# Kernel optimization log

Hardware: AMD Instinct MI355X
Metric: run time of the kernel (lower is better)

## Reference

```python
import jax, jax.numpy as jnp
import numpy as np
import math

V, D, H, L, DFF = 32000, 1024, 16, 4, 4096
B, T_TGT, T_SRC = 4, 512, 512


def setup_inputs() -> dict:
    key = jax.random.key(0)
    ks = iter(jax.random.split(key, 64))
    s = 0.02
    inp = {
        'tgt': jax.random.randint(next(ks), (B, T_TGT), 0, V, dtype=jnp.int32),
        'encoder_output': jax.random.normal(next(ks), (B, T_SRC, D), jnp.float32),
        'tgt_mask': jnp.tril(jnp.ones((T_TGT, T_TGT), jnp.int32)),
        'emb': jax.random.normal(next(ks), (V, D)) * s,
        'Wout': jax.random.normal(next(ks), (D, V)) * s,
        'bout': jnp.zeros((V,)),
    }
    for pfx in ('s', 'c'):  # self / cross attention
        for nm in ('q', 'k', 'v', 'o'):
            inp[f'W{nm}_{pfx}'] = jax.random.normal(next(ks), (L, D, D)) * s
            inp[f'b{nm}_{pfx}'] = jnp.zeros((L, D))
    inp['W1'] = jax.random.normal(next(ks), (L, D, DFF)) * s
    inp['b1'] = jnp.zeros((L, DFF))
    inp['W2'] = jax.random.normal(next(ks), (L, DFF, D)) * s
    inp['b2'] = jnp.zeros((L, D))
    for i in (1, 2, 3):
        inp[f'ln{i}_g'] = jnp.ones((L, D))
        inp[f'ln{i}_b'] = jnp.zeros((L, D))
    return inp


def _layernorm(x, g, b, eps=1e-5):
    m = x.mean(-1, keepdims=True)
    v = ((x - m) ** 2).mean(-1, keepdims=True)
    return g * (x - m) * jax.lax.rsqrt(v + eps) + b


def _mha(xq, xkv, Wq, bq, Wk, bk, Wv, bv, Wo, bo, mask):
    Bq, Tq, Dm = xq.shape
    dk = Dm // H
    q = (xq @ Wq + bq).reshape(Bq, Tq, H, dk).transpose(0, 2, 1, 3)   # bhqd
    k = (xkv @ Wk + bk).reshape(Bq, -1, H, dk).transpose(0, 2, 1, 3)  # bhkd
    v = (xkv @ Wv + bv).reshape(Bq, -1, H, dk).transpose(0, 2, 1, 3)
    scores = jnp.einsum('bhqd,bhkd->bhqk', q, k) / math.sqrt(dk)
    if mask is not None:
        scores = jnp.where(mask[None, None] == 0, -1e9, scores)
    w = jax.nn.softmax(scores, axis=-1)                               # dropout: eval mode
    o = jnp.einsum('bhqk,bhkd->bhqd', w, v).transpose(0, 2, 1, 3).reshape(Bq, Tq, Dm)
    return o @ Wo + bo, w


def _pos_encoding(T, Dm):
    pos = jnp.arange(T, dtype=jnp.float32)[:, None]
    div = jnp.exp(jnp.arange(0, Dm, 2, dtype=jnp.float32) * (-math.log(10000.0) / Dm))
    pe = jnp.zeros((T, Dm))
    pe = pe.at[:, 0::2].set(jnp.sin(pos * div))
    pe = pe.at[:, 1::2].set(jnp.cos(pos * div))
    return pe


def reference(tgt, encoder_output, tgt_mask, emb, Wout, bout,
              Wq_s, bq_s, Wk_s, bk_s, Wv_s, bv_s, Wo_s, bo_s,
              Wq_c, bq_c, Wk_c, bk_c, Wv_c, bv_c, Wo_c, bo_c,
              W1, b1, W2, b2, ln1_g, ln1_b, ln2_g, ln2_b, ln3_g, ln3_b):
    x = emb[tgt] * math.sqrt(D) + _pos_encoding(tgt.shape[1], D)[None]
    self_ws, cross_ws = [], []
    for i in range(L):
        a1, sw = _mha(x, x, Wq_s[i], bq_s[i], Wk_s[i], bk_s[i], Wv_s[i], bv_s[i],
                      Wo_s[i], bo_s[i], tgt_mask)
        x = _layernorm(x + a1, ln1_g[i], ln1_b[i])
        a2, cw = _mha(x, encoder_output, Wq_c[i], bq_c[i], Wk_c[i], bk_c[i],
                      Wv_c[i], bv_c[i], Wo_c[i], bo_c[i], None)
        x = _layernorm(x + a2, ln2_g[i], ln2_b[i])
        ffn = jax.nn.relu(x @ W1[i] + b1[i]) @ W2[i] + b2[i]
        x = _layernorm(x + ffn, ln3_g[i], ln3_b[i])
        self_ws.append(sw)
        cross_ws.append(cw)
    logits = x @ Wout + bout
    return logits, jnp.stack(self_ws), jnp.stack(cross_ws)
```

## Files before the change

kernel.cpp:

```cpp
#include <hip/hip_runtime.h>


typedef unsigned short u16;
typedef __bf16 v8bf __attribute__((ext_vector_type(8)));
typedef float v4f __attribute__((ext_vector_type(4)));

namespace {
constexpr int kB = 4, kT = 512, kD = 1024, kH = 16, kDK = 64, kF = 4096, kV = 32000, kL = 4;
constexpr int kM = kB * kT;
constexpr long kTD = (long)kT * kD;
constexpr long kTT = (long)kT * kT;
constexpr long kHTT = (long)kH * kTT;
constexpr long kBHTT = (long)kB * kHTT;
constexpr long kLOG = (long)kM * kV;
constexpr long kPART = (long)kM * kD;
}

__device__ __forceinline__ u16 f2bf(float f) {
  union { float f; unsigned u; } v; v.f = f;
  unsigned r = v.u + 0x7FFFu + ((v.u >> 16) & 1u);
  return (u16)(r >> 16);
}
__device__ __forceinline__ float bf2f(u16 h) {
  union { unsigned u; float f; } v; v.u = ((unsigned)h) << 16;
  return v.f;
}

typedef __attribute__((address_space(3))) void lds_void;
typedef const __attribute__((address_space(1))) void glob_void;
__device__ __forceinline__ void gl2lds16(const void* g, void* l) {
  __builtin_amdgcn_global_load_lds((glob_void*)g, (lds_void*)l, 16, 0, 0);
}

template <int BM, int BN, int OUTBF, int VTR>
__global__ __launch_bounds__(256)
void gemm_bf(const u16* __restrict__ A0, const u16* __restrict__ B0,
             const float* __restrict__ bias, void* __restrict__ Cv,
             u16* __restrict__ vtw,
             const int K, const int lda, const int ldb, const int ldc,
             const int nH, const long sAb, const long sAh,
             const long sBb, const long sBh, const long sCb, const long sCh,
             const float scale, const int relu, const int bstride) {
  static_assert(BM % 32 == 0 && BN % 32 == 0, "tiles");
  __shared__ u16 As[2][BM][64];
  __shared__ u16 Bs[2][BN][64];
  const int tid = threadIdx.x;
  const int lane = tid & 63;
  const int w = tid >> 6;
  const int z = blockIdx.z;
  const int zb = z / nH, zh = z - zb * nH;
  const u16* A = A0 + zb * sAb + zh * sAh + (long)blockIdx.y * BM * lda;
  const u16* B = B0 + zb * sBb + zh * sBh + (long)blockIdx.x * BN * ldb;
  const long offC = zb * sCb + zh * sCh;
  const int wm = w >> 1, wn = w & 1;
  constexpr int FM = BM / 32, FN = BN / 32;
  v4f acc[FM][FN];
  const v4f zero = {0.f, 0.f, 0.f, 0.f};
#pragma unroll
  for (int i = 0; i < FM; ++i)
#pragma unroll
    for (int j = 0; j < FN; ++j) acc[i][j] = zero;
  const int l15 = lane & 15, lk = lane >> 4;
  const int lr8 = lane >> 3;
  const int swz = ((lane & 7) ^ lr8) * 8;
  const int l7 = l15 & 7;

#pragma unroll
  for (int s = 0; s < BM / 32; ++s)
    gl2lds16(A + (long)(w * (BM / 4) + s * 8 + lr8) * lda + swz,
             &As[0][w * (BM / 4) + s * 8][0]);
#pragma unroll
  for (int s = 0; s < BN / 32; ++s)
    gl2lds16(B + (long)(w * (BN / 4) + s * 8 + lr8) * ldb + swz,
             &Bs[0][w * (BN / 4) + s * 8][0]);

  const int NT = K >> 6;
  for (int kt = 0; kt < NT; ++kt) {
    const int cur = kt & 1;
    __syncthreads();
    if (kt + 1 < NT) {
      const int k0 = (kt + 1) << 6;
#pragma unroll
      for (int s = 0; s < BM / 32; ++s)
        gl2lds16(A + (long)(w * (BM / 4) + s * 8 + lr8) * lda + k0 + swz,
                 &As[cur ^ 1][w * (BM / 4) + s * 8][0]);
#pragma unroll
      for (int s = 0; s < BN / 32; ++s)
        gl2lds16(B + (long)(w * (BN / 4) + s * 8 + lr8) * ldb + k0 + swz,
                 &Bs[cur ^ 1][w * (BN / 4) + s * 8][0]);
    }
#pragma unroll
    for (int t = 0; t < 2; ++t) {
      const int c0 = t * 4;
      v8bf af[FM], bfr[FN];
#pragma unroll
      for (int i = 0; i < FM; ++i)
        af[i] = *(const v8bf*)&As[cur][wm * (BM / 2) + i * 16 + l15][((c0 + lk) ^ l7) * 8];
#pragma unroll
      for (int j = 0; j < FN; ++j)
        bfr[j] = *(const v8bf*)&Bs[cur][wn * (BN / 2) + j * 16 + l15][((c0 + lk) ^ l7) * 8];
#pragma unroll
      for (int i = 0; i < FM; ++i)
#pragma unroll
        for (int j = 0; j < FN; ++j)
          acc[i][j] = __builtin_amdgcn_mfma_f32_16x16x32_bf16(af[i], bfr[j], acc[i][j], 0, 0, 0);
    }
  }

  const long m0 = (long)blockIdx.y * BM + wm * (BM / 2);
  const int n0 = blockIdx.x * BN + wn * (BN / 2);
#pragma unroll
  for (int j = 0; j < FN; ++j) {
    const int col = n0 + j * 16 + l15;
    const float bv = (bias && zb == 0) ? bias[zh * bstride + col] : 0.0f;
#pragma unroll
    for (int i = 0; i < FM; ++i) {
      const long row = m0 + i * 16 + lk * 4;
#pragma unroll
      for (int r = 0; r < 4; ++r) {
        float v = acc[i][j][r] * scale + bv;
        if (relu) v = fmaxf(v, 0.0f);
        const long idx = offC + (row + r) * ldc + col;
        if (OUTBF) ((u16*)Cv)[idx] = f2bf(v);
        else       ((float*)Cv)[idx] = v;
        if (VTR) {
          const int colS = (int)(offC % 3072) + col;
          if (colS >= 2048) {
            const int hh = (colS - 2048) >> 6, dd = (colS - 2048) & 63;
            const int rowg = (int)(row + r);
            vtw[((long)((rowg >> 9) * 16 + hh)) * 32768 + dd * 512 + (rowg & 511)] = f2bf(v);
          }
        }
      }
    }
  }
}

template <int CAUSAL>
__global__ __launch_bounds__(512)
void attn_fused(const u16* __restrict__ Qb, const u16* __restrict__ Kb,
                const u16* __restrict__ vtp, float* __restrict__ wout,
                u16* __restrict__ oout) {
  __shared__ __align__(16) char lds[81920];
  u16 (*Qs)[64] = (u16 (*)[64])lds;
  u16 (*Ks)[64] = (u16 (*)[64])(lds + 16384);
  u16 (*Pl)[136] = (u16 (*)[136])lds;
  u16 (*Vt)[136] = (u16 (*)[136])(lds + 34816);
  __shared__ float redM[128][4];
  __shared__ float redS[128][4];
  const int tid = threadIdx.x, lane = tid & 63, w = tid >> 6;
  const int wm = w >> 2, wn = w & 3;
  const int l15 = lane & 15, lk = lane >> 4;
  const int lr8 = lane >> 3;
  const int swz = ((lane & 7) ^ lr8) * 8;
  const int l7 = l15 & 7;
  const int bx = blockIdx.x;
  const int z = blockIdx.y, zb = z >> 4, zh = z & 15;
  const u16* Q = Qb + (long)zb * 512 * 3072 + zh * 64 + (long)bx * 128 * 3072;
  const u16* Kp = Kb + (long)zb * 512 * 3072 + zh * 64;
  const u16* vtz = vtp + (long)((zb << 4) + zh) * 32768;
  const long obase = (long)zb * kHTT + (long)zh * kTT;

#pragma unroll
  for (int s = 0; s < 2; ++s)
    gl2lds16(Q + (long)(w * 16 + s * 8 + lr8) * 3072 + swz, &Qs[w * 16 + s * 8][0]);
#pragma unroll
  for (int s = 0; s < 8; ++s) {
    const int r0 = w * 64 + s * 8;
    if (!CAUSAL || r0 <= bx * 128 + 127)
      gl2lds16(Kp + (long)(r0 + lr8) * 3072 + swz, &Ks[r0][0]);
  }
  __syncthreads();

  v4f acc[4][8];
  const v4f zero = {0.f, 0.f, 0.f, 0.f};
#pragma unroll
  for (int i = 0; i < 4; ++i)
#pragma unroll
    for (int j = 0; j < 8; ++j) acc[i][j] = zero;

#pragma unroll
  for (int t = 0; t < 2; ++t) {
    const int c0 = t * 4;
    v8bf aq[4], bk[8];
#pragma unroll
    for (int i = 0; i < 4; ++i)
      aq[i] = *(const v8bf*)&Qs[wm * 64 + i * 16 + l15][((c0 + lk) ^ l7) * 8];
#pragma unroll
    for (int j = 0; j < 8; ++j)
      bk[j] = *(const v8bf*)&Ks[wn * 128 + j * 16 + l15][((c0 + lk) ^ l7) * 8];
#pragma unroll
    for (int i = 0; i < 4; ++i)
#pragma unroll
      for (int j = 0; j < 8; ++j)
        if (!(CAUSAL && wn * 128 + j * 16 > bx * 128 + wm * 64 + i * 16 + 15))
          acc[i][j] = __builtin_amdgcn_mfma_f32_16x16x32_bf16(aq[i], bk[j], acc[i][j], 0, 0, 0);
  }

  float gmax[4][4];
#pragma unroll
  for (int i = 0; i < 4; ++i)
#pragma unroll
    for (int r = 0; r < 4; ++r) {
      const int q = bx * 128 + wm * 64 + i * 16 + lk * 4 + r;
      float m = -3.0e38f;
#pragma unroll
      for (int j = 0; j < 8; ++j) {
        const int col = wn * 128 + j * 16 + l15;
        if (!CAUSAL || col <= q) m = fmaxf(m, acc[i][j][r] * 0.125f);
      }
#pragma unroll
      for (int off = 1; off < 16; off <<= 1) m = fmaxf(m, __shfl_xor(m, off));
      if (l15 == 0) redM[wm * 64 + i * 16 + lk * 4 + r][wn] = m;
    }
  __syncthreads();
#pragma unroll
  for (int i = 0; i < 4; ++i)
#pragma unroll
    for (int r = 0; r < 4; ++r) {
      v4f mv = *(const v4f*)&redM[wm * 64 + i * 16 + lk * 4 + r][0];
      gmax[i][r] = fmaxf(fmaxf(mv[0], mv[1]), fmaxf(mv[2], mv[3]));
    }
#pragma unroll
  for (int i = 0; i < 4; ++i)
#pragma unroll
    for (int r = 0; r < 4; ++r) {
      const int q = bx * 128 + wm * 64 + i * 16 + lk * 4 + r;
      float s = 0.0f;
#pragma unroll
      for (int j = 0; j < 8; ++j) {
        const int col = wn * 128 + j * 16 + l15;
        float e = (!CAUSAL || col <= q) ? __expf(acc[i][j][r] * 0.125f - gmax[i][r]) : 0.0f;
        acc[i][j][r] = e;
        s += e;
      }
#pragma unroll
      for (int off = 1; off < 16; off <<= 1) s += __shfl_xor(s, off);
      if (l15 == 0) redS[wm * 64 + i * 16 + lk * 4 + r][wn] = s;
    }
  __syncthreads();
#pragma unroll
  for (int i = 0; i < 4; ++i)
#pragma unroll
    for (int r = 0; r < 4; ++r) {
      v4f sv = *(const v4f*)&redS[wm * 64 + i * 16 + lk * 4 + r][0];
      const float inv = 1.0f / (sv[0] + sv[1] + sv[2] + sv[3]);
      const int q = bx * 128 + wm * 64 + i * 16 + lk * 4 + r;
      const long rowoff = obase + (long)q * 512;
#pragma unroll
      for (int j = 0; j < 8; ++j) {
        const int col = wn * 128 + j * 16 + l15;
        const float v = acc[i][j][r] * inv;
        acc[i][j][r] = v;
        wout[rowoff + col] = v;
      }
    }

  v4f acco[4];
#pragma unroll
  for (int i = 0; i < 4; ++i) acco[i] = zero;
  const int kcMax = CAUSAL ? bx : 3;
  for (int kc = 0; kc <= kcMax; ++kc) {
    __syncthreads();
    if (wn == kc) {
#pragma unroll
      for (int i = 0; i < 4; ++i)
#pragma unroll
        for (int j = 0; j < 8; ++j) {
          const int colk = j * 16 + l15;
#pragma unroll
          for (int r = 0; r < 4; ++r)
            Pl[wm * 64 + i * 16 + lk * 4 + r][colk] = f2bf(acc[i][j][r]);
        }
    }
#pragma unroll
    for (int s = 0; s < 2; ++s) {
      const int c = tid * 2 + s;
      const int d = c >> 4, off = (c & 15) * 8;
      uint4 vv = *(const uint4*)(vtz + (long)d * 512 + kc * 128 + off);
      *(uint4*)&Vt[d][off] = vv;
    }
    __syncthreads();
#pragma unroll
    for (int t = 0; t < 4; ++t) {
      v8bf bv = *(const v8bf*)&Vt[wn * 16 + l15][t * 32 + lk * 8];
#pragma unroll
      for (int i = 0; i < 4; ++i) {
        v8bf ap = *(const v8bf*)&Pl[wm * 64 + i * 16 + l15][t * 32 + lk * 8];
        acco[i] = __builtin_amdgcn_mfma_f32_16x16x32_bf16(ap, bv, acco[i], 0, 0, 0);
      }
    }
  }
#pragma unroll
  for (int i = 0; i < 4; ++i)
#pragma unroll
    for (int r = 0; r < 4; ++r) {
      const int row = bx * 128 + wm * 64 + i * 16 + lk * 4 + r;
      oout[(long)(zb * 512 + row) * 1024 + zh * 64 + wn * 16 + l15] = f2bf(acco[i][r]);
    }
}

struct TPtrs { const float* in[8]; u16* out[8]; };

__global__ void transpose_wt_v2(TPtrs ps, int K, int N) {
  __shared__ float tile[32][33];
  const float* in = ps.in[blockIdx.z];
  u16* o = ps.out[blockIdx.z];
  const int n0 = blockIdx.x * 32, k0 = blockIdx.y * 32;
  const int tx = threadIdx.x, ty = threadIdx.y;
#pragma unroll
  for (int i = 0; i < 4; ++i)
    tile[ty + 8 * i][tx] = in[(long)(k0 + ty + 8 * i) * N + n0 + tx];
  __syncthreads();
#pragma unroll
  for (int i = 0; i < 4; ++i)
    o[(long)(n0 + ty + 8 * i) * K + k0 + tx] = f2bf(tile[tx][ty + 8 * i]);
}

__global__ void concat_bias(float* __restrict__ dst, const float* __restrict__ s0,
                            const float* __restrict__ s1, const float* __restrict__ s2,
                            const int nsrc) {
  const int idx = blockIdx.x * 256 + threadIdx.x;
  const int per = nsrc << 10;
  const int l = idx / per, rem = idx - l * per, s = rem >> 10, j = rem & 1023;
  const float* src = (s == 0) ? s0 : (s == 1 ? s1 : s2);
  dst[idx] = src[l * 1024 + j];
}

__global__ void cvt_bf16_v3(const float* __restrict__ in, u16* __restrict__ o1,
                            u16* __restrict__ o2) {
  const long i = ((long)blockIdx.x * 256 + threadIdx.x) * 4;
  float4 v = *(const float4*)(in + i);
  u16 h[4] = {f2bf(v.x), f2bf(v.y), f2bf(v.z), f2bf(v.w)};
  *(uint2*)(o1 + i) = *(const uint2*)h;
  *(uint2*)(o2 + i) = *(const uint2*)h;
}

__global__ void embed_v2(const int* __restrict__ tgt, const float* __restrict__ emb,
                         float* __restrict__ x, u16* __restrict__ xb) {
  const int row = blockIdx.x;
  const int t = row & (kT - 1);
  const int tok = tgt[row];
  const int c = threadIdx.x * 4;
  float4 e = *(const float4*)(emb + (long)tok * kD + c);
  const float nl = -9.210340371976184f / (float)kD;
  const float a0 = (float)t * expf((float)c * nl);
  const float a1 = (float)t * expf((float)(c + 2) * nl);
  float4 o;
  o.x = e.x * 32.0f + sinf(a0);
  o.y = e.y * 32.0f + cosf(a0);
  o.z = e.z * 32.0f + sinf(a1);
  o.w = e.w * 32.0f + cosf(a1);
  *(float4*)(x + (long)row * kD + c) = o;
  u16 h[4] = {f2bf(o.x), f2bf(o.y), f2bf(o.z), f2bf(o.w)};
  *(uint2*)(xb + (long)row * kD + c) = *(const uint2*)h;
}

__global__ void add_ln_v3(float* __restrict__ x, u16* __restrict__ xb,
                          const float* __restrict__ res, const int nres,
                          const float* __restrict__ g, const float* __restrict__ b) {
  const int row = blockIdx.x;
  const int c = threadIdx.x * 4;
  float4 xv = *(const float4*)(x + (long)row * kD + c);
  float v0 = xv.x, v1 = xv.y, v2 = xv.z, v3 = xv.w;
  for (int p = 0; p < nres; ++p) {
    float4 rv = *(const float4*)(res + p * kPART + (long)row * kD + c);
    v0 += rv.x; v1 += rv.y; v2 += rv.z; v3 += rv.w;
  }
  float s = v0 + v1 + v2 + v3;
  float ss = v0 * v0 + v1 * v1 + v2 * v2 + v3 * v3;
#pragma unroll
  for (int o = 32; o > 0; o >>= 1) { s += __shfl_xor(s, o); ss += __shfl_xor(ss, o); }
  __shared__ float red[4][2];
  const int wv = threadIdx.x >> 6;
  if ((threadIdx.x & 63) == 0) { red[wv][0] = s; red[wv][1] = ss; }
  __syncthreads();
  s  = red[0][0] + red[1][0] + red[2][0] + red[3][0];
  ss = red[0][1] + red[1][1] + red[2][1] + red[3][1];
  const float mean = s * (1.0f / kD);
  const float var = ss * (1.0f / kD) - mean * mean;
  const float rs = rsqrtf(var + 1e-5f);
  float4 gv = *(const float4*)(g + c);
  float4 bv = *(const float4*)(b + c);
  float4 o;
  o.x = gv.x * (v0 - mean) * rs + bv.x;
  o.y = gv.y * (v1 - mean) * rs + bv.y;
  o.z = gv.z * (v2 - mean) * rs + bv.z;
  o.w = gv.w * (v3 - mean) * rs + bv.w;
  *(float4*)(x + (long)row * kD + c) = o;
  u16 h[4] = {f2bf(o.x), f2bf(o.y), f2bf(o.z), f2bf(o.w)};
  *(uint2*)(xb + (long)row * kD + c) = *(const uint2*)h;
}

template <int BM, int BN, typename TA, typename TB, int BKN>
__global__ __launch_bounds__(256)
void gemm_kernel(const void* __restrict__ Av, const void* __restrict__ Bv,
                 const float* __restrict__ bias, float* __restrict__ Cv,
                 const int K, const int lda, const int ldb, const int ldc,
                 const int nH, const long sAb, const long sAh,
                 const long sBb, const long sBh, const long sCb, const long sCh,
                 const float scale, const int relu) {
  constexpr int LP = 40;
  __shared__ u16 As[BM][LP];
  __shared__ u16 Bs[BN][LP];
  const int tid = threadIdx.x;
  const int z = blockIdx.z;
  const int zb = z / nH, zh = z - zb * nH;
  const TA* A = (const TA*)Av + zb * sAb + zh * sAh + (long)blockIdx.y * BM * lda;
  const TB* Bp;
  if constexpr (BKN)
    Bp = (const TB*)Bv + zb * sBb + zh * sBh + (long)blockIdx.x * BN;
  else
    Bp = (const TB*)Bv + zb * sBb + zh * sBh + (long)blockIdx.x * BN * ldb;
  const long offC = zb * sCb + zh * sCh;
  const int lane = tid & 63;
  const int wm = (tid >> 7) & 1, wn = (tid >> 6) & 1;
  constexpr int FM = BM / 32, FN = BN / 32;
  v4f acc[FM][FN];
  const v4f zero = {0.f, 0.f, 0.f, 0.f};
#pragma unroll
  for (int i = 0; i < FM; ++i)
#pragma unroll
    for (int j = 0; j < FN; ++j) acc[i][j] = zero;
  const int l15 = lane & 15, lk = lane >> 4;

  for (int k0 = 0; k0 < K; k0 += 32) {
    __syncthreads();
    if constexpr (sizeof(TA) == 4) {
      const int r = tid >> 3, c = (tid & 7) * 4;
#pragma unroll
      for (int rr = 0; rr < BM; rr += 32) {
        float4 vv = *(const float4*)((const float*)A + (long)(rr + r) * lda + k0 + c);
        unsigned lo = (unsigned)f2bf(vv.x) | ((unsigned)f2bf(vv.y) << 16);
        unsigned hi = (unsigned)f2bf(vv.z) | ((unsigned)f2bf(vv.w) << 16);
        *(uint2*)&As[rr + r][c] = make_uint2(lo, hi);
      }
    } else {
      const int r = tid >> 2, c = (tid & 3) * 8;
#pragma unroll
      for (int rr = 0; rr < BM; rr += 64) {
        uint4 vv = *(const uint4*)((const u16*)A + (long)(rr + r) * lda + k0 + c);
        *(uint4*)&As[rr + r][c] = vv;
      }
    }
    if constexpr (BKN) {
      const int r = tid >> 3, c = (tid & 7) * 4;
#pragma unroll
      for (int nn = 0; nn < BN; nn += 32) {
        float4 vv = *(const float4*)((const float*)Bp + (long)(k0 + r) * ldb + nn + c);
        Bs[nn + c + 0][r] = f2bf(vv.x);
        Bs[nn + c + 1][r] = f2bf(vv.y);
        Bs[nn + c + 2][r] = f2bf(vv.z);
        Bs[nn + c + 3][r] = f2bf(vv.w);
      }
    } else if constexpr (sizeof(TB) == 4) {
      const int r = tid >> 3, c = (tid & 7) * 4;
#pragma unroll
      for (int rr = 0; rr < BN; rr += 32) {
        float4 vv = *(const float4*)((const float*)Bp + (long)(rr + r) * ldb + k0 + c);
        unsigned lo = (unsigned)f2bf(vv.x) | ((unsigned)f2bf(vv.y) << 16);
        unsigned hi = (unsigned)f2bf(vv.z) | ((unsigned)f2bf(vv.w) << 16);
        *(uint2*)&Bs[rr + r][c] = make_uint2(lo, hi);
      }
    } else {
      const int r = tid >> 2, c = (tid & 3) * 8;
#pragma unroll
      for (int rr = 0; rr < BN; rr += 64) {
        uint4 vv = *(const uint4*)((const u16*)Bp + (long)(rr + r) * ldb + k0 + c);
        *(uint4*)&Bs[rr + r][c] = vv;
      }
    }
    __syncthreads();
    v8bf af[FM], bfr[FN];
#pragma unroll
    for (int i = 0; i < FM; ++i)
      af[i] = *(const v8bf*)&As[wm * (BM / 2) + i * 16 + l15][lk * 8];
#pragma unroll
    for (int j = 0; j < FN; ++j)
      bfr[j] = *(const v8bf*)&Bs[wn * (BN / 2) + j * 16 + l15][lk * 8];
#pragma unroll
    for (int i = 0; i < FM; ++i)
#pragma unroll
      for (int j = 0; j < FN; ++j)
        acc[i][j] = __builtin_amdgcn_mfma_f32_16x16x32_bf16(af[i], bfr[j], acc[i][j], 0, 0, 0);
  }

  const long m0 = (long)blockIdx.y * BM + wm * (BM / 2);
  const int n0 = blockIdx.x * BN + wn * (BN / 2);
#pragma unroll
  for (int j = 0; j < FN; ++j) {
    const int col = n0 + j * 16 + l15;
    const float bv = bias ? bias[col] : 0.0f;
#pragma unroll
    for (int i = 0; i < FM; ++i) {
      const long row = m0 + i * 16 + lk * 4;
#pragma unroll
      for (int r = 0; r < 4; ++r) {
        float v = acc[i][j][r] * scale + bv;
        if (relu) v = fmaxf(v, 0.0f);
        Cv[offC + (row + r) * ldc + col] = v;
      }
    }
  }
}

__global__ void embed_kernel(const int* __restrict__ tgt, const float* __restrict__ emb,
                             float* __restrict__ x) {
  const int row = blockIdx.x;
  const int t = row & (kT - 1);
  const int tok = tgt[row];
  const int c = threadIdx.x * 4;
  float4 e = *(const float4*)(emb + (long)tok * kD + c);
  const float nl = -9.210340371976184f / (float)kD;
  const float a0 = (float)t * expf((float)c * nl);
  const float a1 = (float)t * expf((float)(c + 2) * nl);
  float4 o;
  o.x = e.x * 32.0f + sinf(a0);
  o.y = e.y * 32.0f + cosf(a0);
  o.z = e.z * 32.0f + sinf(a1);
  o.w = e.w * 32.0f + cosf(a1);
  *(float4*)(x + (long)row * kD + c) = o;
}

__global__ void transpose_v_kernel(const float* __restrict__ v, u16* __restrict__ vt) {
  __shared__ float tile[32][33];
  const int z = blockIdx.z;
  const int b = z >> 4, h = z & 15;
  const int t0 = blockIdx.x * 32, d0 = blockIdx.y * 32;
  const int tx = threadIdx.x, ty = threadIdx.y;
  const float* in = v + (long)b * kTD + (long)h * kDK;
#pragma unroll
  for (int i = 0; i < 4; ++i)
    tile[ty + 8 * i][tx] = in[(long)(t0 + ty + 8 * i) * kD + d0 + tx];
  __syncthreads();
  u16* o = vt + (long)z * kDK * kT;
#pragma unroll
  for (int i = 0; i < 4; ++i)
    o[(long)(d0 + ty + 8 * i) * kT + t0 + tx] = f2bf(tile[tx][ty + 8 * i]);
}

__global__ void softmax_kernel(float* __restrict__ w, const int causal) {
  const int rowg = blockIdx.x * 4 + (threadIdx.x >> 6);
  const int lane = threadIdx.x & 63;
  const int q = rowg & (kT - 1);
  float* p = w + (long)rowg * kT + lane * 8;
  float4 v0 = *(const float4*)p;
  float4 v1 = *(const float4*)(p + 4);
  float f[8] = {v0.x, v0.y, v0.z, v0.w, v1.x, v1.y, v1.z, v1.w};
  const int base = lane * 8;
  float mx = -3.0e38f;
#pragma unroll
  for (int j = 0; j < 8; ++j)
    if (!causal || base + j <= q) mx = fmaxf(mx, f[j]);
#pragma unroll
  for (int o = 32; o > 0; o >>= 1) mx = fmaxf(mx, __shfl_xor(mx, o));
  float s = 0.0f;
#pragma unroll
  for (int j = 0; j < 8; ++j) {
    float e = (!causal || base + j <= q) ? __expf(f[j] - mx) : 0.0f;
    f[j] = e; s += e;
  }
#pragma unroll
  for (int o = 32; o > 0; o >>= 1) s += __shfl_xor(s, o);
  const float inv = 1.0f / s;
  float4 o0 = {f[0] * inv, f[1] * inv, f[2] * inv, f[3] * inv};
  float4 o1 = {f[4] * inv, f[5] * inv, f[6] * inv, f[7] * inv};
  *(float4*)p = o0;
  *(float4*)(p + 4) = o1;
}

__global__ void add_ln_kernel(float* __restrict__ x, const float* __restrict__ res,
                              const float* __restrict__ g, const float* __restrict__ b) {
  const int row = blockIdx.x;
  const int c = threadIdx.x * 4;
  float4 xv = *(const float4*)(x + (long)row * kD + c);
  float4 rv = *(const float4*)(res + (long)row * kD + c);
  const float v0 = xv.x + rv.x, v1 = xv.y + rv.y, v2 = xv.z + rv.z, v3 = xv.w + rv.w;
  float s = v0 + v1 + v2 + v3;
  float ss = v0 * v0 + v1 * v1 + v2 * v2 + v3 * v3;
#pragma unroll
  for (int o = 32; o > 0; o >>= 1) { s += __shfl_xor(s, o); ss += __shfl_xor(ss, o); }
  __shared__ float red[4][2];
  const int wv = threadIdx.x >> 6;
  if ((threadIdx.x & 63) == 0) { red[wv][0] = s; red[wv][1] = ss; }
  __syncthreads();
  s  = red[0][0] + red[1][0] + red[2][0] + red[3][0];
  ss = red[0][1] + red[1][1] + red[2][1] + red[3][1];
  const float mean = s * (1.0f / kD);
  const float var = ss * (1.0f / kD) - mean * mean;
  const float rs = rsqrtf(var + 1e-5f);
  float4 gv = *(const float4*)(g + c);
  float4 bv = *(const float4*)(b + c);
  float4 o;
  o.x = gv.x * (v0 - mean) * rs + bv.x;
  o.y = gv.y * (v1 - mean) * rs + bv.y;
  o.z = gv.z * (v2 - mean) * rs + bv.z;
  o.w = gv.w * (v3 - mean) * rs + bv.w;
  *(float4*)(x + (long)row * kD + c) = o;
}

extern "C" void kernel_launch(void* const* d_in, const int* in_sizes, int n_in,
                              void* d_out, int out_size, void* d_ws, size_t ws_size,
                              hipStream_t stream) {
  const int*   tgt  = (const int*)d_in[0];
  const float* enc  = (const float*)d_in[1];
  const float* emb  = (const float*)d_in[3];
  const float* Wout = (const float*)d_in[4];
  const float* bout = (const float*)d_in[5];
  const float* Wq_s = (const float*)d_in[6];
  const float* bq_s = (const float*)d_in[7];
  const float* Wk_s = (const float*)d_in[8];
  const float* bk_s = (const float*)d_in[9];
  const float* Wv_s = (const float*)d_in[10];
  const float* bv_s = (const float*)d_in[11];
  const float* Wo_s = (const float*)d_in[12];
  const float* bo_s = (const float*)d_in[13];
  const float* Wq_c = (const float*)d_in[14];
  const float* bq_c = (const float*)d_in[15];
  const float* Wk_c = (const float*)d_in[16];
  const float* bk_c = (const float*)d_in[17];
  const float* Wv_c = (const float*)d_in[18];
  const float* bv_c = (const float*)d_in[19];
  const float* Wo_c = (const float*)d_in[20];
  const float* bo_c = (const float*)d_in[21];
  const float* W1   = (const float*)d_in[22];
  const float* b1   = (const float*)d_in[23];
  const float* W2   = (const float*)d_in[24];
  const float* b2   = (const float*)d_in[25];
  const float* ln1g = (const float*)d_in[26];
  const float* ln1b = (const float*)d_in[27];
  const float* ln2g = (const float*)d_in[28];
  const float* ln2b = (const float*)d_in[29];
  const float* ln3g = (const float*)d_in[30];
  const float* ln3b = (const float*)d_in[31];

  float* out = (float*)d_out;
  const long DD = (long)kD * kD;
  const dim3 blk256(256), blkT(32, 8);

  if (ws_size >= (272ll << 20)) {
    char* ws = (char*)d_ws;
    float* x     = (float*)ws;
    u16* xb      = (u16*)(ws + (8l << 20));
    u16* encb    = (u16*)(ws + (12l << 20));
    u16* encb2   = (u16*)(ws + (16l << 20));
    u16* Sqkv    = (u16*)(ws + (20l << 20));
    u16* vt      = (u16*)(ws + (32l << 20));
    u16* S3b     = (u16*)(ws + (36l << 20));
    u16* Hb      = (u16*)(ws + (40l << 20));
    float* Spart = (float*)(ws + (56l << 20));
    u16* wbase   = (u16*)(ws + (72l << 20));
    u16* woutT   = (u16*)(ws + (200l << 20));
    float* bqkvS = (float*)(ws + (263l << 20));
    float* bqkvC = (float*)(ws + (263l << 20) + (64l << 10));
    const long WLAY = 16l * 1024 * 1024;

    for (int i = 0; i < kL; ++i) {
      u16* wqkvS = wbase + i * WLAY;
      u16* woS   = wqkvS + 3072 * 1024;
      u16* wqkvC = woS + 1024 * 1024;
      u16* woC   = wqkvC + 3072 * 1024;
      u16* w1t   = woC + 1024 * 1024;
      u16* w2t   = w1t + (long)4096 * 1024;
      TPtrs p{};
      p.in[0] = Wq_s + i * DD; p.out[0] = wqkvS;
      p.in[1] = Wk_s + i * DD; p.out[1] = wqkvS + 1024 * 1024;
      p.in[2] = Wv_s + i * DD; p.out[2] = wqkvS + 2048 * 1024;
      p.in[3] = Wo_s + i * DD; p.out[3] = woS;
      p.in[4] = Wq_c + i * DD; p.out[4] = wqkvC;
      p.in[5] = Wk_c + i * DD; p.out[5] = wqkvC + 1024 * 1024;
      p.in[6] = Wv_c + i * DD; p.out[6] = wqkvC + 2048 * 1024;
      p.in[7] = Wo_c + i * DD; p.out[7] = woC;
      transpose_wt_v2<<<dim3(32, 32, 8), blkT, 0, stream>>>(p, 1024, 1024);
      TPtrs p1{}; p1.in[0] = W1 + (long)i * kD * kF; p1.out[0] = w1t;
      transpose_wt_v2<<<dim3(128, 32, 1), blkT, 0, stream>>>(p1, 1024, 4096);
      TPtrs p2{}; p2.in[0] = W2 + (long)i * kF * kD; p2.out[0] = w2t;
      transpose_wt_v2<<<dim3(32, 128, 1), blkT, 0, stream>>>(p2, 4096, 1024);
    }
    TPtrs po{}; po.in[0] = Wout; po.out[0] = woutT;
    transpose_wt_v2<<<dim3(1000, 32, 1), blkT, 0, stream>>>(po, 1024, 32000);
    concat_bias<<<dim3(48), blk256, 0, stream>>>(bqkvS, bq_s, bk_s, bv_s, 3);
    concat_bias<<<dim3(48), blk256, 0, stream>>>(bqkvC, bq_c, bk_c, bv_c, 3);
    cvt_bf16_v3<<<dim3(2048), blk256, 0, stream>>>(enc, encb, encb2);
    embed_v2<<<dim3(kM), blk256, 0, stream>>>(tgt, emb, x, xb);

    for (int i = 0; i < kL; ++i) {
      u16* wqkvS = wbase + i * WLAY;
      u16* woS   = wqkvS + 3072 * 1024;
      u16* wqkvC = woS + 1024 * 1024;
      u16* woC   = wqkvC + 3072 * 1024;
      u16* w1t   = woC + 1024 * 1024;
      u16* w2t   = w1t + (long)4096 * 1024;
      float* wSelf  = out + kLOG + (long)i * kBHTT;
      float* wCross = out + kLOG + (long)kL * kBHTT + (long)i * kBHTT;

      gemm_bf<128, 128, 1, 1><<<dim3(24, 16, 1), blk256, 0, stream>>>(
          xb, wqkvS, bqkvS + i * 3072, Sqkv, vt, 1024, 1024, 1024, 3072,
          1, 0, 0, 0, 0, 0, 0, 1.0f, 0, 0);
      attn_fused<1><<<dim3(4, 64), dim3(512), 0, stream>>>(Sqkv, Sqkv + 1024, vt, wSelf, S3b);
      gemm_bf<128, 128, 0, 0><<<dim3(8, 16, 2), blk256, 0, stream>>>(
          S3b, woS, bo_s + (long)i * kD, Spart, nullptr, 512, 1024, 1024, 1024,
          1, 512, 0, 512, 0, kPART, 0, 1.0f, 0, 0);
      add_ln_v3<<<dim3(kM), blk256, 0, stream>>>(x, xb, Spart, 2,
          ln1g + (long)i * kD, ln1b + (long)i * kD);

      gemm_bf<128, 128, 1, 1><<<dim3(8, 16, 3), blk256, 0, stream>>>(
          xb, wqkvC, bqkvC + i * 3072, Sqkv, vt, 1024, 1024, 1024, 3072,
          3, 0, (long)2048 * 1024, 0, (long)1024 * 1024, 0, 1024, 1.0f, 0, 1024);
      attn_fused<0><<<dim3(4, 64), dim3(512), 0, stream>>>(Sqkv, Sqkv + 1024, vt, wCross, S3b);
      gemm_bf<128, 128, 0, 0><<<dim3(8, 16, 2), blk256, 0, stream>>>(
          S3b, woC, bo_c + (long)i * kD, Spart, nullptr, 512, 1024, 1024, 1024,
          1, 512, 0, 512, 0, kPART, 0, 1.0f, 0, 0);
      add_ln_v3<<<dim3(kM), blk256, 0, stream>>>(x, xb, Spart, 2,
          ln2g + (long)i * kD, ln2b + (long)i * kD);

      gemm_bf<128, 128, 1, 0><<<dim3(32, 16, 1), blk256, 0, stream>>>(
          xb, w1t, b1 + (long)i * kF, Hb, nullptr, 1024, 1024, 1024, 4096,
          1, 0, 0, 0, 0, 0, 0, 1.0f, 1, 0);
      gemm_bf<128, 128, 0, 0><<<dim3(8, 16, 2), blk256, 0, stream>>>(
          Hb, w2t, b2 + (long)i * kD, Spart, nullptr, 2048, 4096, 4096, 1024,
          1, 2048, 0, 2048, 0, kPART, 0, 1.0f, 0, 0);
      add_ln_v3<<<dim3(kM), blk256, 0, stream>>>(x, xb, Spart, 2,
          ln3g + (long)i * kD, ln3b + (long)i * kD);
    }

    gemm_bf<128, 128, 0, 0><<<dim3(250, 16, 1), blk256, 0, stream>>>(
        xb, woutT, bout, out, nullptr, 1024, 1024, 1024, 32000,
        1, 0, 0, 0, 0, 0, 0, 1.0f, 0, 0);
    return;
  }

  float* x = (float*)d_ws;
  char* sc = (char*)d_out;
  float* S0 = (float*)sc;
  float* S1 = (float*)(sc + (8l  << 20));
  float* S2 = (float*)(sc + (16l << 20));
  float* S3 = (float*)(sc + (24l << 20));
  float* S4 = (float*)(sc + (32l << 20));
  u16*   vt = (u16*)  (sc + (40l << 20));

  embed_kernel<<<dim3(kM), blk256, 0, stream>>>(tgt, emb, x);
  auto wgemm = [&](const float* A, const float* W, const float* bias, float* C) {
    gemm_kernel<128, 128, float, float, 1><<<dim3(kD / 128, kM / 128, 1), blk256, 0, stream>>>(
        A, W, bias, C, kD, kD, kD, kD, 1, 0, 0, 0, 0, 0, 0, 1.0f, 0);
  };
  for (int i = 0; i < kL; ++i) {
    const long wOff = (long)i * DD;
    float* wSelf  = out + kLOG + (long)i * kBHTT;
    float* wCross = out + kLOG + (long)kL * kBHTT + (long)i * kBHTT;
    wgemm(x, Wq_s + wOff, bq_s + (long)i * kD, S0);
    wgemm(x, Wk_s + wOff, bk_s + (long)i * kD, S1);
    wgemm(x, Wv_s + wOff, bv_s + (long)i * kD, S2);
    transpose_v_kernel<<<dim3(16, 2, 64), blkT, 0, stream>>>(S2, vt);
    gemm_kernel<128, 128, float, float, 0><<<dim3(4, 4, 64), blk256, 0, stream>>>(
        S0, S1, nullptr, wSelf, kDK, kD, kD, kT,
        kH, kTD, (long)kDK, kTD, (long)kDK, kHTT, kTT, 0.125f, 0);
    softmax_kernel<<<dim3(kB * kH * kT / 4), blk256, 0, stream>>>(wSelf, 1);
    gemm_kernel<128, 64, float, u16, 0><<<dim3(1, 4, 64), blk256, 0, stream>>>(
        wSelf, vt, nullptr, S3, kT, kT, kT, kD,
        kH, kHTT, kTT, (long)kH * kDK * kT, (long)kDK * kT, kTD, (long)kDK, 1.0f, 0);
    wgemm(S3, Wo_s + wOff, bo_s + (long)i * kD, S0);
    add_ln_kernel<<<dim3(kM), blk256, 0, stream>>>(x, S0, ln1g + (long)i * kD, ln1b + (long)i * kD);
    wgemm(x,   Wq_c + wOff, bq_c + (long)i * kD, S0);
    wgemm(enc, Wk_c + wOff, bk_c + (long)i * kD, S1);
    wgemm(enc, Wv_c + wOff, bv_c + (long)i * kD, S2);
    transpose_v_kernel<<<dim3(16, 2, 64), blkT, 0, stream>>>(S2, vt);
    gemm_kernel<128, 128, float, float, 0><<<dim3(4, 4, 64), blk256, 0, stream>>>(
        S0, S1, nullptr, wCross, kDK, kD, kD, kT,
        kH, kTD, (long)kDK, kTD, (long)kDK, kHTT, kTT, 0.125f, 0);
    softmax_kernel<<<dim3(kB * kH * kT / 4), blk256, 0, stream>>>(wCross, 0);
    gemm_kernel<128, 64, float, u16, 0><<<dim3(1, 4, 64), blk256, 0, stream>>>(
        wCross, vt, nullptr, S3, kT, kT, kT, kD,
        kH, kHTT, kTT, (long)kH * kDK * kT, (long)kDK * kT, kTD, (long)kDK, 1.0f, 0);
    wgemm(S3, Wo_c + wOff, bo_c + (long)i * kD, S0);
    add_ln_kernel<<<dim3(kM), blk256, 0, stream>>>(x, S0, ln2g + (long)i * kD, ln2b + (long)i * kD);
    gemm_kernel<128, 128, float, float, 1><<<dim3(kF / 128, kM / 128, 1), blk256, 0, stream>>>(
        x, W1 + (long)i * kD * kF, b1 + (long)i * kF, S0, kD, kD, kF, kF,
        1, 0, 0, 0, 0, 0, 0, 1.0f, 1);
    gemm_kernel<128, 128, float, float, 1><<<dim3(kD / 128, kM / 128, 1), blk256, 0, stream>>>(
        S0, W2 + (long)i * kF * kD, b2 + (long)i * kD, S4, kF, kF, kD, kD,
        1, 0, 0, 0, 0, 0, 0, 1.0f, 0);
    add_ln_kernel<<<dim3(kM), blk256, 0, stream>>>(x, S4, ln3g + (long)i * kD, ln3b + (long)i * kD);
  }
  gemm_kernel<128, 128, float, float, 1><<<dim3(kV / 128, kM / 128, 1), blk256, 0, stream>>>(
      x, Wout, bout, out, kD, kD, kV, kV,
      1, 0, 0, 0, 0, 0, 0, 1.0f, 0);
}
```

Before: 1.534 ms.

## Deepen split-K for N=1024 GEMMs with single-buffer variant; vectorize weight transpose

The output-projection and FFN-down GEMMs now use 4-way split-K instead of 2-way, and the layernorm kernels sum four partials. These split-K launches use a new single-buffered GEMM variant that halves LDS per block, aiming for higher occupancy at the cost of losing load/compute overlap. The weight transpose moves to 64x64 tiles with float4 loads and 8-byte stores to cut transpose time. Workspace offsets grow to fit the larger partial-sum buffer, which raises the workspace threshold for the fast path.

```diff
diff --git a/kernel.cpp b/kernel.cpp
--- a/kernel.cpp
+++ b/kernel.cpp
@@ -32,7 +32,7 @@
   __builtin_amdgcn_global_load_lds((glob_void*)g, (lds_void*)l, 16, 0, 0);
 }
 
-template <int BM, int BN, int OUTBF, int VTR>
+template <int BM, int BN, int OUTBF, int VTR, int DBUF>
 __global__ __launch_bounds__(256)
 void gemm_bf(const u16* __restrict__ A0, const u16* __restrict__ B0,
              const float* __restrict__ bias, void* __restrict__ Cv,
@@ -42,8 +42,8 @@
              const long sBb, const long sBh, const long sCb, const long sCh,
              const float scale, const int relu, const int bstride) {
   static_assert(BM % 32 == 0 && BN % 32 == 0, "tiles");
-  __shared__ u16 As[2][BM][64];
-  __shared__ u16 Bs[2][BN][64];
+  __shared__ u16 As[DBUF + 1][BM][64];
+  __shared__ u16 Bs[DBUF + 1][BN][64];
   const int tid = threadIdx.x;
   const int lane = tid & 63;
   const int w = tid >> 6;
@@ -65,45 +65,76 @@
   const int swz = ((lane & 7) ^ lr8) * 8;
   const int l7 = l15 & 7;
 
-#pragma unroll
-  for (int s = 0; s < BM / 32; ++s)
-    gl2lds16(A + (long)(w * (BM / 4) + s * 8 + lr8) * lda + swz,
-             &As[0][w * (BM / 4) + s * 8][0]);
-#pragma unroll
-  for (int s = 0; s < BN / 32; ++s)
-    gl2lds16(B + (long)(w * (BN / 4) + s * 8 + lr8) * ldb + swz,
-             &Bs[0][w * (BN / 4) + s * 8][0]);
-
-  const int NT = K >> 6;
-  for (int kt = 0; kt < NT; ++kt) {
-    const int cur = kt & 1;
-    __syncthreads();
-    if (kt + 1 < NT) {
-      const int k0 = (kt + 1) << 6;
+  if constexpr (DBUF) {
+#pragma unroll
+    for (int s = 0; s < BM / 32; ++s)
+      gl2lds16(A + (long)(w * (BM / 4) + s * 8 + lr8) * lda + swz,
+               &As[0][w * (BM / 4) + s * 8][0]);
+#pragma unroll
+    for (int s = 0; s < BN / 32; ++s)
+      gl2lds16(B + (long)(w * (BN / 4) + s * 8 + lr8) * ldb + swz,
+               &Bs[0][w * (BN / 4) + s * 8][0]);
+
+    const int NT = K >> 6;
+    for (int kt = 0; kt < NT; ++kt) {
+      const int cur = kt & 1;
+      __syncthreads();
+      if (kt + 1 < NT) {
+        const int k0 = (kt + 1) << 6;
+#pragma unroll
+        for (int s = 0; s < BM / 32; ++s)
+          gl2lds16(A + (long)(w * (BM / 4) + s * 8 + lr8) * lda + k0 + swz,
+                   &As[cur ^ 1][w * (BM / 4) + s * 8][0]);
+#pragma unroll
+        for (int s = 0; s < BN / 32; ++s)
+          gl2lds16(B + (long)(w * (BN / 4) + s * 8 + lr8) * ldb + k0 + swz,
+                   &Bs[cur ^ 1][w * (BN / 4) + s * 8][0]);
+      }
+#pragma unroll
+      for (int t = 0; t < 2; ++t) {
+        const int c0 = t * 4;
+        v8bf af[FM], bfr[FN];
+#pragma unroll
+        for (int i = 0; i < FM; ++i)
+          af[i] = *(const v8bf*)&As[cur][wm * (BM / 2) + i * 16 + l15][((c0 + lk) ^ l7) * 8];
+#pragma unroll
+        for (int j = 0; j < FN; ++j)
+          bfr[j] = *(const v8bf*)&Bs[cur][wn * (BN / 2) + j * 16 + l15][((c0 + lk) ^ l7) * 8];
+#pragma unroll
+        for (int i = 0; i < FM; ++i)
+#pragma unroll
+          for (int j = 0; j < FN; ++j)
+            acc[i][j] = __builtin_amdgcn_mfma_f32_16x16x32_bf16(af[i], bfr[j], acc[i][j], 0, 0, 0);
+      }
+    }
+  } else {
+    for (int k0 = 0; k0 < K; k0 += 64) {
+      __syncthreads();
 #pragma unroll
       for (int s = 0; s < BM / 32; ++s)
         gl2lds16(A + (long)(w * (BM / 4) + s * 8 + lr8) * lda + k0 + swz,
-                 &As[cur ^ 1][w * (BM / 4) + s * 8][0]);
+                 &As[0][w * (BM / 4) + s * 8][0]);
 #pragma unroll
       for (int s = 0; s < BN / 32; ++s)
         gl2lds16(B + (long)(w * (BN / 4) + s * 8 + lr8) * ldb + k0 + swz,
-                 &Bs[cur ^ 1][w * (BN / 4) + s * 8][0]);
-    }
-#pragma unroll
-    for (int t = 0; t < 2; ++t) {
-      const int c0 = t * 4;
-      v8bf af[FM], bfr[FN];
-#pragma unroll
-      for (int i = 0; i < FM; ++i)
-        af[i] = *(const v8bf*)&As[cur][wm * (BM / 2) + i * 16 + l15][((c0 + lk) ^ l7) * 8];
-#pragma unroll
-      for (int j = 0; j < FN; ++j)
-        bfr[j] = *(const v8bf*)&Bs[cur][wn * (BN / 2) + j * 16 + l15][((c0 + lk) ^ l7) * 8];
-#pragma unroll
-      for (int i = 0; i < FM; ++i)
+                 &Bs[0][w * (BN / 4) + s * 8][0]);
+      __syncthreads();
+#pragma unroll
+      for (int t = 0; t < 2; ++t) {
+        const int c0 = t * 4;
+        v8bf af[FM], bfr[FN];
+#pragma unroll
+        for (int i = 0; i < FM; ++i)
+          af[i] = *(const v8bf*)&As[0][wm * (BM / 2) + i * 16 + l15][((c0 + lk) ^ l7) * 8];
 #pragma unroll
         for (int j = 0; j < FN; ++j)
-          acc[i][j] = __builtin_amdgcn_mfma_f32_16x16x32_bf16(af[i], bfr[j], acc[i][j], 0, 0, 0);
+          bfr[j] = *(const v8bf*)&Bs[0][wn * (BN / 2) + j * 16 + l15][((c0 + lk) ^ l7) * 8];
+#pragma unroll
+        for (int i = 0; i < FM; ++i)
+#pragma unroll
+          for (int j = 0; j < FN; ++j)
+            acc[i][j] = __builtin_amdgcn_mfma_f32_16x16x32_bf16(af[i], bfr[j], acc[i][j], 0, 0, 0);
+      }
     }
   }
 
@@ -302,19 +333,30 @@
 
 struct TPtrs { const float* in[8]; u16* out[8]; };
 
-__global__ void transpose_wt_v2(TPtrs ps, int K, int N) {
-  __shared__ float tile[32][33];
+__global__ void transpose_wt_v3(TPtrs ps, int K, int N) {
+  __shared__ float tile[64][65];
   const float* in = ps.in[blockIdx.z];
   u16* o = ps.out[blockIdx.z];
-  const int n0 = blockIdx.x * 32, k0 = blockIdx.y * 32;
-  const int tx = threadIdx.x, ty = threadIdx.y;
-#pragma unroll
-  for (int i = 0; i < 4; ++i)
-    tile[ty + 8 * i][tx] = in[(long)(k0 + ty + 8 * i) * N + n0 + tx];
+  const int n0 = blockIdx.x * 64, k0 = blockIdx.y * 64;
+  const int tr = threadIdx.x >> 4;
+  const int tc = (threadIdx.x & 15) * 4;
+#pragma unroll
+  for (int i = 0; i < 4; ++i) {
+    float4 v = *(const float4*)(in + (long)(k0 + tr + 16 * i) * N + n0 + tc);
+    tile[tr + 16 * i][tc + 0] = v.x;
+    tile[tr + 16 * i][tc + 1] = v.y;
+    tile[tr + 16 * i][tc + 2] = v.z;
+    tile[tr + 16 * i][tc + 3] = v.w;
+  }
   __syncthreads();
 #pragma unroll
-  for (int i = 0; i < 4; ++i)
-    o[(long)(n0 + ty + 8 * i) * K + k0 + tx] = f2bf(tile[tx][ty + 8 * i]);
+  for (int i = 0; i < 4; ++i) {
+    const int rr = tr + 16 * i;
+    u16 h[4];
+#pragma unroll
+    for (int j = 0; j < 4; ++j) h[j] = f2bf(tile[tc + j][rr]);
+    *(uint2*)(o + (long)(n0 + rr) * K + k0 + tc) = *(const uint2*)h;
+  }
 }
 
 __global__ void concat_bias(float* __restrict__ dst, const float* __restrict__ s0,
@@ -638,7 +680,7 @@
   const long DD = (long)kD * kD;
   const dim3 blk256(256), blkT(32, 8);
 
-  if (ws_size >= (272ll << 20)) {
+  if (ws_size >= (320ll << 20)) {
     char* ws = (char*)d_ws;
     float* x     = (float*)ws;
     u16* xb      = (u16*)(ws + (8l << 20));
@@ -649,10 +691,10 @@
     u16* S3b     = (u16*)(ws + (36l << 20));
     u16* Hb      = (u16*)(ws + (40l << 20));
     float* Spart = (float*)(ws + (56l << 20));
-    u16* wbase   = (u16*)(ws + (72l << 20));
-    u16* woutT   = (u16*)(ws + (200l << 20));
-    float* bqkvS = (float*)(ws + (263l << 20));
-    float* bqkvC = (float*)(ws + (263l << 20) + (64l << 10));
+    u16* wbase   = (u16*)(ws + (88l << 20));
+    u16* woutT   = (u16*)(ws + (216l << 20));
+    float* bqkvS = (float*)(ws + (280l << 20));
+    float* bqkvC = (float*)(ws + (280l << 20) + (64l << 10));
     const long WLAY = 16l * 1024 * 1024;
 
     for (int i = 0; i < kL; ++i) {
@@ -671,14 +713,14 @@
       p.in[5] = Wk_c + i * DD; p.out[5] = wqkvC + 1024 * 1024;
       p.in[6] = Wv_c + i * DD; p.out[6] = wqkvC + 2048 * 1024;
       p.in[7] = Wo_c + i * DD; p.out[7] = woC;
-      transpose_wt_v2<<<dim3(32, 32, 8), blkT, 0, stream>>>(p, 1024, 1024);
+      transpose_wt_v3<<<dim3(16, 16, 8), blk256, 0, stream>>>(p, 1024, 1024);
       TPtrs p1{}; p1.in[0] = W1 + (long)i * kD * kF; p1.out[0] = w1t;
-      transpose_wt_v2<<<dim3(128, 32, 1), blkT, 0, stream>>>(p1, 1024, 4096);
+      transpose_wt_v3<<<dim3(64, 16, 1), blk256, 0, stream>>>(p1, 1024, 4096);
       TPtrs p2{}; p2.in[0] = W2 + (long)i * kF * kD; p2.out[0] = w2t;
-      transpose_wt_v2<<<dim3(32, 128, 1), blkT, 0, stream>>>(p2, 4096, 1024);
+      transpose_wt_v3<<<dim3(16, 64, 1), blk256, 0, stream>>>(p2, 4096, 1024);
     }
     TPtrs po{}; po.in[0] = Wout; po.out[0] = woutT;
-    transpose_wt_v2<<<dim3(1000, 32, 1), blkT, 0, stream>>>(po, 1024, 32000);
+    transpose_wt_v3<<<dim3(500, 16, 1), blk256, 0, stream>>>(po, 1024, 32000);
     concat_bias<<<dim3(48), blk256, 0, stream>>>(bqkvS, bq_s, bk_s, bv_s, 3);
     concat_bias<<<dim3(48), blk256, 0, stream>>>(bqkvC, bq_c, bk_c, bv_c, 3);
     cvt_bf16_v3<<<dim3(2048), blk256, 0, stream>>>(enc, encb, encb2);
@@ -694,37 +736,37 @@
       float* wSelf  = out + kLOG + (long)i * kBHTT;
       float* wCross = out + kLOG + (long)kL * kBHTT + (long)i * kBHTT;
 
-      gemm_bf<128, 128, 1, 1><<<dim3(24, 16, 1), blk256, 0, stream>>>(
+      gemm_bf<128, 128, 1, 1, 1><<<dim3(24, 16, 1), blk256, 0, stream>>>(
           xb, wqkvS, bqkvS + i * 3072, Sqkv, vt, 1024, 1024, 1024, 3072,
           1, 0, 0, 0, 0, 0, 0, 1.0f, 0, 0);
       attn_fused<1><<<dim3(4, 64), dim3(512), 0, stream>>>(Sqkv, Sqkv + 1024, vt, wSelf, S3b);
-      gemm_bf<128, 128, 0, 0><<<dim3(8, 16, 2), blk256, 0, stream>>>(
-          S3b, woS, bo_s + (long)i * kD, Spart, nullptr, 512, 1024, 1024, 1024,
-          1, 512, 0, 512, 0, kPART, 0, 1.0f, 0, 0);
-      add_ln_v3<<<dim3(kM), blk256, 0, stream>>>(x, xb, Spart, 2,
+      gemm_bf<128, 128, 0, 0, 0><<<dim3(8, 16, 4), blk256, 0, stream>>>(
+          S3b, woS, bo_s + (long)i * kD, Spart, nullptr, 256, 1024, 1024, 1024,
+          1, 256, 0, 256, 0, kPART, 0, 1.0f, 0, 0);
+      add_ln_v3<<<dim3(kM), blk256, 0, stream>>>(x, xb, Spart, 4,
           ln1g + (long)i * kD, ln1b + (long)i * kD);
 
-      gemm_bf<128, 128, 1, 1><<<dim3(8, 16, 3), blk256, 0, stream>>>(
+      gemm_bf<128, 128, 1, 1, 1><<<dim3(8, 16, 3), blk256, 0, stream>>>(
           xb, wqkvC, bqkvC + i * 3072, Sqkv, vt, 1024, 1024, 1024, 3072,
           3, 0, (long)2048 * 1024, 0, (long)1024 * 1024, 0, 1024, 1.0f, 0, 1024);
       attn_fused<0><<<dim3(4, 64), dim3(512), 0, stream>>>(Sqkv, Sqkv + 1024, vt, wCross, S3b);
-      gemm_bf<128, 128, 0, 0><<<dim3(8, 16, 2), blk256, 0, stream>>>(
-          S3b, woC, bo_c + (long)i * kD, Spart, nullptr, 512, 1024, 1024, 1024,
-          1, 512, 0, 512, 0, kPART, 0, 1.0f, 0, 0);
-      add_ln_v3<<<dim3(kM), blk256, 0, stream>>>(x, xb, Spart, 2,
+      gemm_bf<128, 128, 0, 0, 0><<<dim3(8, 16, 4), blk256, 0, stream>>>(
+          S3b, woC, bo_c + (long)i * kD, Spart, nullptr, 256, 1024, 1024, 1024,
+          1, 256, 0, 256, 0, kPART, 0, 1.0f, 0, 0);
+      add_ln_v3<<<dim3(kM), blk256, 0, stream>>>(x, xb, Spart, 4,
           ln2g + (long)i * kD, ln2b + (long)i * kD);
 
-      gemm_bf<128, 128, 1, 0><<<dim3(32, 16, 1), blk256, 0, stream>>>(
+      gemm_bf<128, 128, 1, 0, 1><<<dim3(32, 16, 1), blk256, 0, stream>>>(
           xb, w1t, b1 + (long)i * kF, Hb, nullptr, 1024, 1024, 1024, 4096,
           1, 0, 0, 0, 0, 0, 0, 1.0f, 1, 0);
-      gemm_bf<128, 128, 0, 0><<<dim3(8, 16, 2), blk256, 0, stream>>>(
-          Hb, w2t, b2 + (long)i * kD, Spart, nullptr, 2048, 4096, 4096, 1024,
-          1, 2048, 0, 2048, 0, kPART, 0, 1.0f, 0, 0);
-      add_ln_v3<<<dim3(kM), blk256, 0, stream>>>(x, xb, Spart, 2,
+      gemm_bf<128, 128, 0, 0, 0><<<dim3(8, 16, 4), blk256, 0, stream>>>(
+          Hb, w2t, b2 + (long)i * kD, Spart, nullptr, 1024, 4096, 4096, 1024,
+          1, 1024, 0, 1024, 0, kPART, 0, 1.0f, 0, 0);
+      add_ln_v3<<<dim3(kM), blk256, 0, stream>>>(x, xb, Spart, 4,
           ln3g + (long)i * kD, ln3b + (long)i * kD);
     }
 
-    gemm_bf<128, 128, 0, 0><<<dim3(250, 16, 1), blk256, 0, stream>>>(
+    gemm_bf<128, 128, 0, 0, 1><<<dim3(250, 16, 1), blk256, 0, stream>>>(
         xb, woutT, bout, out, nullptr, 1024, 1024, 1024, 32000,
         1, 0, 0, 0, 0, 0, 0, 1.0f, 0, 0);
     return;
```

After: 1.512 ms. About the same (-1.4%).
